# Kernel tuning notes

Hardware: AMD Instinct MI355X
Metric: run time of the kernel (lower is better)

## Reference

```python
import jax, jax.numpy as jnp
import numpy as np
from itertools import combinations

M, N = 20, 4                      # modes, photons -> dim = C(23,4) = 8855
MODES = (0, 1)                    # detected modes
VALUES = [(a, b) for a in range(N + 1) for b in range(N + 1 - a)]  # 15 outcomes
B = 4                             # batch of density matrices


def _photon_basis(m, n):
    """All Fock states of n photons in m modes (stars and bars), shape [dim, m]."""
    states = []
    slots = n + m - 1
    for bars in combinations(range(slots), m - 1):
        prev, state = -1, []
        for b in list(bars) + [slots]:
            state.append(b - prev - 1)
            prev = b
        states.append(state)
    return np.array(states, dtype=np.int64)


def _projector():
    """0/1 indicator matrix [dim, n_values]: P[i, j] = 1 iff basis state i matches outcome j on detected modes."""
    basis = _photon_basis(M, N)                       # [dim, m]
    sub = basis[:, list(MODES)]                       # [dim, 2]
    vals = np.array(VALUES, dtype=np.int64)           # [n_values, 2]
    P = (sub[:, None, :] == vals[None, :, :]).all(-1).astype(np.float32)
    return P


def setup_inputs() -> dict:
    key = jax.random.key(0)
    P = jnp.asarray(_projector())                     # [8855, 15]
    dim = P.shape[0]
    x = jax.random.normal(key, (B, dim, dim), dtype=jnp.float32)
    return {"input": x, "P": P}


def reference(input, P):
    # Original: stack([P.T @ diag(rho) for rho in input]) -> [B, n_values].
    # Vectorized: pull per-sample diagonals, then one small GEMM (segment sum via 0/1 P).
    diag = jnp.diagonal(input, axis1=1, axis2=2)      # [B, dim]
    return diag @ P                                   # [B, n_values]
```

## Files before the change

kernel.cpp:

```cpp
#include <hip/hip_runtime.h>


#define NVAL 15

__global__ void zero_out_kernel(float* out, int n) {
    int t = blockIdx.x * blockDim.x + threadIdx.x;
    if (t < n) out[t] = 0.0f;
}

__global__ __launch_bounds__(256) void diag_proj_kernel(
        const float* __restrict__ x,
        const float* __restrict__ P,
        float* __restrict__ out,
        int dim) {
    __shared__ float bins[NVAL];
    const int t = threadIdx.x;
    if (t < NVAL) bins[t] = 0.0f;
    __syncthreads();

    const int i = blockIdx.x * blockDim.x + t;
    const int b = blockIdx.y;

    if (i < dim) {
        const size_t base = (size_t)b * (size_t)dim * (size_t)dim;
        const float d = x[base + (size_t)i * (size_t)(dim + 1)];

        int j = 0;
        const float* __restrict__ prow = P + (size_t)i * NVAL;
#pragma unroll
        for (int jj = 0; jj < NVAL; ++jj) {
            if (prow[jj] != 0.0f) j = jj;
        }
        atomicAdd(&bins[j], d);
    }
    __syncthreads();

    if (t < NVAL) {
        const float v = bins[t];
        if (v != 0.0f) atomicAdd(&out[b * NVAL + t], v);
    }
}

extern "C" void kernel_launch(void* const* d_in, const int* in_sizes, int n_in,
                              void* d_out, int out_size, void* d_ws, size_t ws_size,
                              hipStream_t stream) {
    const float* x = (const float*)d_in[0];
    const float* P = (const float*)d_in[1];
    float* out = (float*)d_out;

    const int dim = in_sizes[1] / NVAL;
    const int B   = (int)(in_sizes[0] / ((long long)dim * dim));

    zero_out_kernel<<<(out_size + 63) / 64, 64, 0, stream>>>(out, out_size);

    dim3 grid((dim + 255) / 256, B);
    diag_proj_kernel<<<grid, 256, 0, stream>>>(x, P, out, dim);
}
```

Baseline: 1.302 ms.

## Fuse zeroing into one block per batch with register-batched diagonal loads

Drops the separate zeroing kernel and the global atomics. Each batch element is now handled by a single 1024-thread block. Every thread issues up to 9 strided diagonal loads, plus the projector-row scans, before doing its shared-memory atomic adds, and the block writes its 15 bins straight to the output. This removes a launch and the global atomic traffic, but cuts the grid from about 140 blocks to B=4 blocks, so the scattered, latency-bound diagonal loads run on far fewer compute units.

```diff
diff --git a/kernel.cpp b/kernel.cpp
--- a/kernel.cpp
+++ b/kernel.cpp
@@ -2,43 +2,63 @@
 
 
 #define NVAL 15
+#define BLK 1024
+#define KITER 9
 
-__global__ void zero_out_kernel(float* out, int n) {
-    int t = blockIdx.x * blockDim.x + threadIdx.x;
-    if (t < n) out[t] = 0.0f;
-}
-
-__global__ __launch_bounds__(256) void diag_proj_kernel(
+__global__ __launch_bounds__(BLK) void diag_proj_fused(
         const float* __restrict__ x,
         const float* __restrict__ P,
         float* __restrict__ out,
         int dim) {
     __shared__ float bins[NVAL];
     const int t = threadIdx.x;
+    const int b = blockIdx.x;
+
     if (t < NVAL) bins[t] = 0.0f;
     __syncthreads();
 
-    const int i = blockIdx.x * blockDim.x + t;
-    const int b = blockIdx.y;
+    const size_t base   = (size_t)b * (size_t)dim * (size_t)dim;
+    const size_t dstride = (size_t)dim + 1;
 
-    if (i < dim) {
-        const size_t base = (size_t)b * (size_t)dim * (size_t)dim;
-        const float d = x[base + (size_t)i * (size_t)(dim + 1)];
+    float d[KITER];
+    int   j[KITER];
 
-        int j = 0;
+#pragma unroll
+    for (int k = 0; k < KITER; ++k) {
+        const int i = t + k * BLK;
+        if (i < dim) {
+            d[k] = x[base + (size_t)i * dstride];
+            const float* __restrict__ prow = P + (size_t)i * NVAL;
+            int jj = 0;
+#pragma unroll
+            for (int c = 0; c < NVAL; ++c) {
+                if (prow[c] != 0.0f) jj = c;
+            }
+            j[k] = jj;
+        } else {
+            d[k] = 0.0f;
+            j[k] = 0;
+        }
+    }
+
+    for (int i = t + BLK * KITER; i < dim; i += BLK) {
+        const float dv = x[base + (size_t)i * dstride];
         const float* __restrict__ prow = P + (size_t)i * NVAL;
+        int jj = 0;
 #pragma unroll
-        for (int jj = 0; jj < NVAL; ++jj) {
-            if (prow[jj] != 0.0f) j = jj;
+        for (int c = 0; c < NVAL; ++c) {
+            if (prow[c] != 0.0f) jj = c;
         }
-        atomicAdd(&bins[j], d);
+        atomicAdd(&bins[jj], dv);
+    }
+
+#pragma unroll
+    for (int k = 0; k < KITER; ++k) {
+        atomicAdd(&bins[j[k]], d[k]);
     }
     __syncthreads();
 
-    if (t < NVAL) {
-        const float v = bins[t];
-        if (v != 0.0f) atomicAdd(&out[b * NVAL + t], v);
-    }
+    if (t < NVAL) out[b * NVAL + t] = bins[t];
 }
 
 extern "C" void kernel_launch(void* const* d_in, const int* in_sizes, int n_in,
@@ -51,8 +71,5 @@
     const int dim = in_sizes[1] / NVAL;
     const int B   = (int)(in_sizes[0] / ((long long)dim * dim));
 
-    zero_out_kernel<<<(out_size + 63) / 64, 64, 0, stream>>>(out, out_size);
-
-    dim3 grid((dim + 255) / 256, B);
-    diag_proj_kernel<<<grid, 256, 0, stream>>>(x, P, out, dim);
+    diag_proj_fused<<<dim3(B), dim3(BLK), 0, stream>>>(x, P, out, dim);
 }
```

Result: slower. 1.387 ms (+6.5%).
